# Optimization experiments

Measured on AMD Instinct MI355X. Metric: run time of the kernel, lower is better.

Reference implementation:

```python
import jax, jax.numpy as jnp
import numpy as np

H = 128      # hidden_size
ATT = 128    # attention_size
NS = 1024    # num attendee statements
NE = 512     # num attendee eres
M = 1024     # num attenders


def setup_inputs() -> dict:
    key = jax.random.key(0)
    ks = jax.random.split(key, 16)
    s = 1.0 / np.sqrt(H)
    return {
        'attendee_stmts': jax.random.normal(ks[0], (NS, H), jnp.float32),
        'attendee_eres': jax.random.normal(ks[1], (NE, H), jnp.float32),
        'attender': jax.random.normal(ks[2], (M, H), jnp.float32),
        # Score stmt_to_stmt (concat): Linear(2H->H) then Linear(H->1)
        'Wc_s': jax.random.normal(ks[3], (H, 2 * H), jnp.float32) * s,
        'bc_s': jax.random.normal(ks[4], (H,), jnp.float32) * s,
        'ws_s': jax.random.normal(ks[5], (H,), jnp.float32) * s,
        'bs_s': jax.random.normal(ks[6], (1,), jnp.float32) * s,
        # Score ere_to_stmt (concat)
        'Wc_e': jax.random.normal(ks[7], (H, 2 * H), jnp.float32) * s,
        'bc_e': jax.random.normal(ks[8], (H,), jnp.float32) * s,
        'ws_e': jax.random.normal(ks[9], (H,), jnp.float32) * s,
        'bs_e': jax.random.normal(ks[10], (1,), jnp.float32) * s,
        # Attention combine: Linear(3H -> ATT)
        'W_lin': jax.random.normal(ks[11], (ATT, 3 * H), jnp.float32) * s,
        'b_lin': jax.random.normal(ks[12], (ATT,), jnp.float32) * s,
        # coherence_linear: Linear(ATT -> 1)
        'W_coh': jax.random.normal(ks[13], (1, ATT), jnp.float32) * s,
        'b_coh': jax.random.normal(ks[14], (1,), jnp.float32) * s,
    }


def _concat_score(first, second, Wc, bc, ws, bs):
    # torch: single(tanh(concat(cat([first_i, second_j])))) over all (i, j)
    # split concat weight so we never materialize the [N, M, 2H] concat
    h = first.shape[-1]
    A = first @ Wc[:, :h].T + bc          # [N, H]
    B = second @ Wc[:, h:].T              # [M, H]
    Hnm = jnp.tanh(A[:, None, :] + B[None, :, :])   # [N, M, H]
    return jnp.einsum('nmh,h->nm', Hnm, ws) + bs[0]  # [N, M]


def reference(attendee_stmts, attendee_eres, attender,
              Wc_s, bc_s, ws_s, bs_s,
              Wc_e, bc_e, ws_e, bs_e,
              W_lin, b_lin, W_coh, b_coh):
    # unnormalized scores, softmax over attendees (dim 0)
    w_ss = jax.nn.softmax(_concat_score(attendee_stmts, attender, Wc_s, bc_s, ws_s, bs_s), axis=0)  # [NS, M]
    w_es = jax.nn.softmax(_concat_score(attendee_eres, attender, Wc_e, bc_e, ws_e, bs_e), axis=0)   # [NE, M]
    # context vectors: weights^T @ attendees
    ctx_s = jnp.einsum('nm,nh->mh', w_ss, attendee_stmts)  # [M, H]
    ctx_e = jnp.einsum('nm,nh->mh', w_es, attendee_eres)   # [M, H]
    feats = jnp.concatenate([attender, ctx_s, ctx_e], axis=-1)  # [M, 3H]
    att_vec = jnp.tanh(feats @ W_lin.T + b_lin)                 # [M, ATT]
    coherence = att_vec @ W_coh.T + b_coh                       # [M, 1]
    return coherence
```

## Files before the change

### kernel.cpp

```cpp
#include <hip/hip_runtime.h>
#include <math.h>

#define H   128
#define NS  1024
#define NE  512
#define M   1024
#define K2  2.8853900817779268f

__device__ __forceinline__ float exp2_fast(float x) {
#if __has_builtin(__builtin_amdgcn_exp2f)
    return __builtin_amdgcn_exp2f(x);
#else
    return __expf(x * 0.6931471805599453f);
#endif
}

__device__ __forceinline__ float fast_tanh(float x) {
    float e = __expf(2.0f * x);
    float r = __builtin_amdgcn_rcpf(1.0f + e);
    return 1.0f - 2.0f * r;
}

__global__ __launch_bounds__(256) void k_tr(const float* __restrict__ Wc_s,
                                            const float* __restrict__ Wc_e,
                                            const float* __restrict__ W_lin,
                                            float* __restrict__ WT_s1, float* __restrict__ WT_s2,
                                            float* __restrict__ WT_e1, float* __restrict__ WT_e2,
                                            float* __restrict__ WT_lin) {
    int idx = blockIdx.x * 256 + threadIdx.x;
    if (idx < 65536) {
        int t = idx >> 14, r = idx & 16383, k = r >> 7, hh = r & 127;
        const float* src = (t < 2) ? Wc_s : Wc_e;
        int off = (t & 1) * H;
        float v = K2 * src[hh * 256 + off + k];
        float* dst = (t == 0) ? WT_s1 : (t == 1) ? WT_s2 : (t == 2) ? WT_e1 : WT_e2;
        dst[r] = v;
    } else {
        int j2 = idx - 65536;
        int k = j2 >> 7, a = j2 & 127;
        WT_lin[j2] = W_lin[a * 384 + k];
    }
}

__global__ __launch_bounds__(256) void k_proj(const float* __restrict__ stmts,
                                              const float* __restrict__ eres,
                                              const float* __restrict__ attender,
                                              const float* __restrict__ WT_s1,
                                              const float* __restrict__ WT_s2,
                                              const float* __restrict__ WT_e1,
                                              const float* __restrict__ WT_e2,
                                              const float* __restrict__ bc_s,
                                              const float* __restrict__ bc_e,
                                              float* __restrict__ EAT_s, float* __restrict__ EB_s,
                                              float* __restrict__ EAT_e, float* __restrict__ EB_e) {
    __shared__ float xr[16][H];
    __shared__ float red[16][H];
    int b   = blockIdx.x;
    int tid = threadIdx.x;
    int t    = tid & 127;
    int half = tid >> 7;

    if (b < 96) {
        const float *X, *WT, *bias; float* OT; int r0, N;
        if (b < 64) { X = stmts; WT = WT_s1; bias = bc_s; OT = EAT_s; r0 = b * 16;        N = NS; }
        else        { X = eres;  WT = WT_e1; bias = bc_e; OT = EAT_e; r0 = (b - 64) * 16; N = NE; }
        for (int i = tid; i < 16 * H; i += 256) xr[i >> 7][i & 127] = X[(r0 + (i >> 7)) * H + (i & 127)];
        __syncthreads();
        float b0 = (half == 0) ? K2 * bias[t] : 0.0f;
        float acc[16];
        #pragma unroll
        for (int r = 0; r < 16; ++r) acc[r] = b0;
        int k0 = half * 64;
        #pragma unroll 4
        for (int k = k0; k < k0 + 64; ++k) {
            float wv = WT[k * H + t];
            #pragma unroll
            for (int r = 0; r < 16; ++r) acc[r] += xr[r][k] * wv;
        }
        if (half) {
            #pragma unroll
            for (int r = 0; r < 16; ++r) red[r][t] = acc[r];
        }
        __syncthreads();
        if (!half) {
            #pragma unroll
            for (int r = 0; r < 16; ++r) xr[r][t] = exp2_fast(acc[r] + red[r][t]);
        }
        __syncthreads();
        {
            int hh  = tid >> 1;
            int seg = (tid & 1) * 8;
            float4 v0 = make_float4(xr[seg + 0][hh], xr[seg + 1][hh], xr[seg + 2][hh], xr[seg + 3][hh]);
            float4 v1 = make_float4(xr[seg + 4][hh], xr[seg + 5][hh], xr[seg + 6][hh], xr[seg + 7][hh]);
            *(float4*)(OT + (size_t)hh * N + r0 + seg)     = v0;
            *(float4*)(OT + (size_t)hh * N + r0 + seg + 4) = v1;
        }
    } else {
        int b2 = b - 96;
        const float* WT = (b2 < 256) ? WT_s2 : WT_e2;
        float* O        = (b2 < 256) ? EB_s : EB_e;
        int r0          = (b2 & 255) * 4;
        float* xf = &xr[0][0];
        xf[tid]       = attender[r0 * H + tid];
        xf[tid + 256] = attender[r0 * H + 256 + tid];
        __syncthreads();
        float acc[4] = {0.f, 0.f, 0.f, 0.f};
        int k0 = half * 64;
        #pragma unroll 8
        for (int k = k0; k < k0 + 64; ++k) {
            float wv = WT[k * H + t];
            #pragma unroll
            for (int r = 0; r < 4; ++r) acc[r] += xf[r * H + k] * wv;
        }
        if (half) {
            #pragma unroll
            for (int r = 0; r < 4; ++r) red[r][t] = acc[r];
        }
        __syncthreads();
        if (!half) {
            #pragma unroll
            for (int r = 0; r < 4; ++r) O[(r0 + r) * H + t] = exp2_fast(acc[r] + red[r][t]);
        }
    }
}

#define PAIR(eax, eay, ebx, eby, wx, wy, accv)                 \
    { float q0 = fmaf(eax, ebx, 1.0f);                         \
      float q1 = fmaf(eay, eby, 1.0f);                         \
      float nn = wx * q1; nn = fmaf(wy, q0, nn);               \
      float rr = __builtin_amdgcn_rcpf(q0 * q1);               \
      accv = fmaf(nn, rr, accv); }

__global__ __launch_bounds__(512, 4) void k_score_ctx(const float* __restrict__ EAT_s,
                                                      const float* __restrict__ EB_s,
                                                      const float* __restrict__ ws_s,
                                                      const float* __restrict__ EAT_e,
                                                      const float* __restrict__ EB_e,
                                                      const float* __restrict__ ws_e,
                                                      const float* __restrict__ stmts,
                                                      const float* __restrict__ eres,
                                                      float* __restrict__ ctx_s,
                                                      float* __restrict__ ctx_e) {
    __shared__ float Bs[4][H];
    __shared__ float wbuf[1024][4];
    __shared__ float part[4][4][H];
    __shared__ float scrm[8][4], scrs[8][4], rzl[4];

    int b = blockIdx.x;
    bool is_e = (b >= 256);
    int m0 = (is_e ? (b - 256) : b) * 4;
    const float* EAT = is_e ? EAT_e : EAT_s;
    const float* EB  = is_e ? EB_e  : EB_s;
    const float* wsv = is_e ? ws_e  : ws_s;
    const float* X   = is_e ? eres  : stmts;
    float* ctxout    = is_e ? ctx_e : ctx_s;
    int N    = is_e ? NE : NS;
    int ROWS = is_e ? 1 : 2;
    int t = threadIdx.x;

    Bs[t >> 7][t & 127] = EB[(size_t)(m0 + (t >> 7)) * H + (t & 127)];
    __syncthreads();

    float acc[2][4] = {{0.f,0.f,0.f,0.f},{0.f,0.f,0.f,0.f}};
    float a[2][8];
    #pragma unroll
    for (int k = 0; k < 8; ++k) a[0][k] = EAT[(size_t)k * N + t];
    if (ROWS > 1) {
        #pragma unroll
        for (int k = 0; k < 8; ++k) a[1][k] = EAT[(size_t)k * N + t + 512];
    }
    #pragma unroll
    for (int ch = 0; ch < 16; ++ch) {
        int h0 = ch * 8;
        float an[2][8];
        if (ch < 15) {
            #pragma unroll
            for (int k = 0; k < 8; ++k) an[0][k] = EAT[(size_t)(h0 + 8 + k) * N + t];
            if (ROWS > 1) {
                #pragma unroll
                for (int k = 0; k < 8; ++k) an[1][k] = EAT[(size_t)(h0 + 8 + k) * N + t + 512];
            }
        }
        float wv[8];
        #pragma unroll
        for (int k = 0; k < 8; ++k) wv[k] = wsv[h0 + k];
        #pragma unroll
        for (int mj = 0; mj < 4; ++mj) {
            float bv[8];
            #pragma unroll
            for (int k = 0; k < 8; ++k) bv[k] = Bs[mj][h0 + k];
            PAIR(a[0][0], a[0][1], bv[0], bv[1], wv[0], wv[1], acc[0][mj]);
            PAIR(a[0][2], a[0][3], bv[2], bv[3], wv[2], wv[3], acc[0][mj]);
            PAIR(a[0][4], a[0][5], bv[4], bv[5], wv[4], wv[5], acc[0][mj]);
            PAIR(a[0][6], a[0][7], bv[6], bv[7], wv[6], wv[7], acc[0][mj]);
            if (ROWS > 1) {
                PAIR(a[1][0], a[1][1], bv[0], bv[1], wv[0], wv[1], acc[1][mj]);
                PAIR(a[1][2], a[1][3], bv[2], bv[3], wv[2], wv[3], acc[1][mj]);
                PAIR(a[1][4], a[1][5], bv[4], bv[5], wv[4], wv[5], acc[1][mj]);
                PAIR(a[1][6], a[1][7], bv[6], bv[7], wv[6], wv[7], acc[1][mj]);
            }
        }
        if (ch < 15) {
            #pragma unroll
            for (int k = 0; k < 8; ++k) a[0][k] = an[0][k];
            if (ROWS > 1) {
                #pragma unroll
                for (int k = 0; k < 8; ++k) a[1][k] = an[1][k];
            }
        }
    }

    int wave = t >> 6;
    float mx[4];
    for (int mj = 0; mj < 4; ++mj) {
        float v = -2.0f * acc[0][mj];
        if (ROWS > 1) v = fmaxf(v, -2.0f * acc[1][mj]);
        mx[mj] = v;
    }
    #pragma unroll
    for (int off = 32; off > 0; off >>= 1)
        for (int mj = 0; mj < 4; ++mj) mx[mj] = fmaxf(mx[mj], __shfl_xor(mx[mj], off, 64));
    if ((t & 63) == 0) {
        for (int mj = 0; mj < 4; ++mj) scrm[wave][mj] = mx[mj];
    }
    __syncthreads();
    for (int mj = 0; mj < 4; ++mj) {
        float r = scrm[0][mj];
        for (int i = 1; i < 8; ++i) r = fmaxf(r, scrm[i][mj]);
        mx[mj] = r;
    }

    float w0[4], w1[4], sm[4];
    for (int mj = 0; mj < 4; ++mj) {
        w0[mj] = __expf(fmaf(-2.0f, acc[0][mj], -mx[mj]));
        sm[mj] = w0[mj];
        if (ROWS > 1) { w1[mj] = __expf(fmaf(-2.0f, acc[1][mj], -mx[mj])); sm[mj] += w1[mj]; }
    }
    #pragma unroll
    for (int off = 32; off > 0; off >>= 1)
        for (int mj = 0; mj < 4; ++mj) sm[mj] += __shfl_xor(sm[mj], off, 64);
    if ((t & 63) == 0) {
        for (int mj = 0; mj < 4; ++mj) scrs[wave][mj] = sm[mj];
    }

    for (int mj = 0; mj < 4; ++mj) {
        wbuf[t][mj] = w0[mj];
        if (ROWS > 1) wbuf[t + 512][mj] = w1[mj];
    }
    __syncthreads();
    if (t < 4) {
        float s = scrs[0][t];
        for (int i = 1; i < 8; ++i) s += scrs[i][t];
        rzl[t] = __builtin_amdgcn_rcpf(s);
    }
    __syncthreads();

    {
        int h = t & 127;
        int g = t >> 7;
        int CH = N >> 2;
        const float* Xb = X + (size_t)(g * CH) * H + h;
        const float* wb = &wbuf[g * CH][0];
        float cacc[4] = {0.f, 0.f, 0.f, 0.f};
        #pragma unroll 8
        for (int nn = 0; nn < CH; ++nn) {
            float x = Xb[(size_t)nn * H];
            float4 w4 = *(const float4*)(wb + nn * 4);
            cacc[0] += w4.x * x; cacc[1] += w4.y * x;
            cacc[2] += w4.z * x; cacc[3] += w4.w * x;
        }
        #pragma unroll
        for (int mj = 0; mj < 4; ++mj) part[g][mj][h] = cacc[mj];
    }
    __syncthreads();
    {
        int mj = t >> 7, h = t & 127;
        float s = part[0][mj][h] + part[1][mj][h] + part[2][mj][h] + part[3][mj][h];
        ctxout[(size_t)(m0 + mj) * H + h] = s * rzl[mj];
    }
}

__global__ __launch_bounds__(512) void k_mlp(const float* __restrict__ attender,
                                             const float* __restrict__ ctx_s,
                                             const float* __restrict__ ctx_e,
                                             const float* __restrict__ WT_lin,
                                             const float* __restrict__ b_lin,
                                             const float* __restrict__ W_coh,
                                             const float* __restrict__ b_coh,
                                             float* __restrict__ out) {
    __shared__ float feats[4][3 * H];
    __shared__ float red2[8];
    int m0 = blockIdx.x * 4;
    int t  = threadIdx.x;

    for (int i = t; i < 4 * 3 * H; i += 512) {
        int r = i / (3 * H), c = i % (3 * H);
        float v;
        if (c < H)            v = attender[(size_t)(m0 + r) * H + c];
        else if (c < 2 * H)   v = ctx_s[(size_t)(m0 + r) * H + (c - H)];
        else                  v = ctx_e[(size_t)(m0 + r) * H + (c - 2 * H)];
        feats[r][c] = v;
    }
    __syncthreads();

    int a  = t & 127;
    int jm = t >> 7;
    float acc = b_lin[a];
    #pragma unroll 8
    for (int k = 0; k < 3 * H; ++k)
        acc += feats[jm][k] * WT_lin[k * H + a];
    float v = fast_tanh(acc) * W_coh[a];
    #pragma unroll
    for (int off = 32; off > 0; off >>= 1) v += __shfl_down(v, off, 64);
    if ((t & 63) == 0) red2[t >> 6] = v;
    __syncthreads();
    if (t < 4) out[m0 + t] = red2[2 * t] + red2[2 * t + 1] + b_coh[0];
}

extern "C" void kernel_launch(void* const* d_in, const int* in_sizes, int n_in,
                              void* d_out, int out_size, void* d_ws, size_t ws_size,
                              hipStream_t stream) {
    const float* stmts    = (const float*)d_in[0];
    const float* eres     = (const float*)d_in[1];
    const float* attender = (const float*)d_in[2];
    const float* Wc_s     = (const float*)d_in[3];
    const float* bc_s     = (const float*)d_in[4];
    const float* ws_s     = (const float*)d_in[5];
    const float* Wc_e     = (const float*)d_in[7];
    const float* bc_e     = (const float*)d_in[8];
    const float* ws_e     = (const float*)d_in[9];
    const float* W_lin    = (const float*)d_in[11];
    const float* b_lin    = (const float*)d_in[12];
    const float* W_coh    = (const float*)d_in[13];
    const float* b_coh    = (const float*)d_in[14];
    float* out = (float*)d_out;

    float* ws    = (float*)d_ws;
    float* WT_s1 = ws;
    float* WT_s2 = WT_s1 + H * H;
    float* WT_e1 = WT_s2 + H * H;
    float* WT_e2 = WT_e1 + H * H;
    float* WT_li = WT_e2 + H * H;
    float* EAT_s = WT_li + 3 * H * H;
    float* EB_s  = EAT_s + NS * H;
    float* EAT_e = EB_s + M * H;
    float* EB_e  = EAT_e + NE * H;
    float* c_s   = EB_e + M * H;
    float* c_e   = c_s + (size_t)M * H;

    k_tr<<<448, 256, 0, stream>>>(Wc_s, Wc_e, W_lin, WT_s1, WT_s2, WT_e1, WT_e2, WT_li);
    k_proj<<<608, 256, 0, stream>>>(stmts, eres, attender, WT_s1, WT_s2, WT_e1, WT_e2,
                                    bc_s, bc_e, EAT_s, EB_s, EAT_e, EB_e);
    k_score_ctx<<<512, 512, 0, stream>>>(EAT_s, EB_s, ws_s, EAT_e, EB_e, ws_e,
                                         stmts, eres, c_s, c_e);
    k_mlp<<<M / 4, 512, 0, stream>>>(attender, c_s, c_e, WT_li, b_lin, W_coh, b_coh, out);
}
```

Measured before the change: 67.88 us.

## Halve attenders per block in score kernel to double grid and occupancy

Each score/context block now handles 2 attenders instead of 4, so the grid grows from 512 to 1024 blocks and the launch bound asks for 8 blocks per CU. The shared-memory staging of the attender projection is removed, and B values are read straight from global memory (uniform loads). The software prefetch of the next EAT chunk is also dropped. The aim is more parallelism and lower register and LDS pressure. In exchange, each EAT element is reloaded twice as often across blocks, and the exp/rcp work per loaded element falls, which lowers arithmetic intensity.

Result: slower. 76.52 us (+12.7%).

```diff
diff --git a/kernel.cpp b/kernel.cpp
--- a/kernel.cpp
+++ b/kernel.cpp
@@ -131,7 +131,7 @@
       float rr = __builtin_amdgcn_rcpf(q0 * q1);               \
       accv = fmaf(nn, rr, accv); }
 
-__global__ __launch_bounds__(512, 4) void k_score_ctx(const float* __restrict__ EAT_s,
+__global__ __launch_bounds__(512, 8) void k_score_ctx(const float* __restrict__ EAT_s,
                                                       const float* __restrict__ EB_s,
                                                       const float* __restrict__ ws_s,
                                                       const float* __restrict__ EAT_e,
@@ -141,14 +141,13 @@
                                                       const float* __restrict__ eres,
                                                       float* __restrict__ ctx_s,
                                                       float* __restrict__ ctx_e) {
-    __shared__ float Bs[4][H];
-    __shared__ float wbuf[1024][4];
-    __shared__ float part[4][4][H];
-    __shared__ float scrm[8][4], scrs[8][4], rzl[4];
+    __shared__ float wbuf[1024][2];
+    __shared__ float part[4][2][H];
+    __shared__ float scrm[8][2], scrs[8][2], rzl[2];
 
     int b = blockIdx.x;
-    bool is_e = (b >= 256);
-    int m0 = (is_e ? (b - 256) : b) * 4;
+    bool is_e = (b >= 512);
+    int m0 = (is_e ? (b - 512) : b) * 2;
     const float* EAT = is_e ? EAT_e : EAT_s;
     const float* EB  = is_e ? EB_e  : EB_s;
     const float* wsv = is_e ? ws_e  : ws_s;
@@ -158,97 +157,84 @@
     int ROWS = is_e ? 1 : 2;
     int t = threadIdx.x;
 
-    Bs[t >> 7][t & 127] = EB[(size_t)(m0 + (t >> 7)) * H + (t & 127)];
-    __syncthreads();
-
-    float acc[2][4] = {{0.f,0.f,0.f,0.f},{0.f,0.f,0.f,0.f}};
-    float a[2][8];
-    #pragma unroll
-    for (int k = 0; k < 8; ++k) a[0][k] = EAT[(size_t)k * N + t];
-    if (ROWS > 1) {
-        #pragma unroll
-        for (int k = 0; k < 8; ++k) a[1][k] = EAT[(size_t)k * N + t + 512];
-    }
-    #pragma unroll
+    const float* eb0 = EB + (size_t)m0 * H;
+    const float* eb1 = EB + (size_t)(m0 + 1) * H;
+
+    float acc[2][2] = {{0.f, 0.f}, {0.f, 0.f}};
     for (int ch = 0; ch < 16; ++ch) {
         int h0 = ch * 8;
-        float an[2][8];
-        if (ch < 15) {
-            #pragma unroll
-            for (int k = 0; k < 8; ++k) an[0][k] = EAT[(size_t)(h0 + 8 + k) * N + t];
-            if (ROWS > 1) {
-                #pragma unroll
-                for (int k = 0; k < 8; ++k) an[1][k] = EAT[(size_t)(h0 + 8 + k) * N + t + 512];
-            }
-        }
-        float wv[8];
+        float a0[8], a1[8];
         #pragma unroll
-        for (int k = 0; k < 8; ++k) wv[k] = wsv[h0 + k];
+        for (int k = 0; k < 8; ++k) a0[k] = EAT[(size_t)(h0 + k) * N + t];
+        if (ROWS > 1) {
+            #pragma unroll
+            for (int k = 0; k < 8; ++k) a1[k] = EAT[(size_t)(h0 + k) * N + t + 512];
+        }
+        float wv[8], b0[8], b1[8];
         #pragma unroll
-        for (int mj = 0; mj < 4; ++mj) {
-            float bv[8];
-            #pragma unroll
-            for (int k = 0; k < 8; ++k) bv[k] = Bs[mj][h0 + k];
-            PAIR(a[0][0], a[0][1], bv[0], bv[1], wv[0], wv[1], acc[0][mj]);
-            PAIR(a[0][2], a[0][3], bv[2], bv[3], wv[2], wv[3], acc[0][mj]);
-            PAIR(a[0][4], a[0][5], bv[4], bv[5], wv[4], wv[5], acc[0][mj]);
-            PAIR(a[0][6], a[0][7], bv[6], bv[7], wv[6], wv[7], acc[0][mj]);
-            if (ROWS > 1) {
-                PAIR(a[1][0], a[1][1], bv[0], bv[1], wv[0], wv[1], acc[1][mj]);
-                PAIR(a[1][2], a[1][3], bv[2], bv[3], wv[2], wv[3], acc[1][mj]);
-                PAIR(a[1][4], a[1][5], bv[4], bv[5], wv[4], wv[5], acc[1][mj]);
-                PAIR(a[1][6], a[1][7], bv[6], bv[7], wv[6], wv[7], acc[1][mj]);
-            }
-        }
-        if (ch < 15) {
-            #pragma unroll
-            for (int k = 0; k < 8; ++k) a[0][k] = an[0][k];
-            if (ROWS > 1) {
-                #pragma unroll
-                for (int k = 0; k < 8; ++k) a[1][k] = an[1][k];
-            }
+        for (int k = 0; k < 8; ++k) {
+            wv[k] = wsv[h0 + k];
+            b0[k] = eb0[h0 + k];
+            b1[k] = eb1[h0 + k];
+        }
+        PAIR(a0[0], a0[1], b0[0], b0[1], wv[0], wv[1], acc[0][0]);
+        PAIR(a0[2], a0[3], b0[2], b0[3], wv[2], wv[3], acc[0][0]);
+        PAIR(a0[4], a0[5], b0[4], b0[5], wv[4], wv[5], acc[0][0]);
+        PAIR(a0[6], a0[7], b0[6], b0[7], wv[6], wv[7], acc[0][0]);
+        PAIR(a0[0], a0[1], b1[0], b1[1], wv[0], wv[1], acc[0][1]);
+        PAIR(a0[2], a0[3], b1[2], b1[3], wv[2], wv[3], acc[0][1]);
+        PAIR(a0[4], a0[5], b1[4], b1[5], wv[4], wv[5], acc[0][1]);
+        PAIR(a0[6], a0[7], b1[6], b1[7], wv[6], wv[7], acc[0][1]);
+        if (ROWS > 1) {
+            PAIR(a1[0], a1[1], b0[0], b0[1], wv[0], wv[1], acc[1][0]);
+            PAIR(a1[2], a1[3], b0[2], b0[3], wv[2], wv[3], acc[1][0]);
+            PAIR(a1[4], a1[5], b0[4], b0[5], wv[4], wv[5], acc[1][0]);
+            PAIR(a1[6], a1[7], b0[6], b0[7], wv[6], wv[7], acc[1][0]);
+            PAIR(a1[0], a1[1], b1[0], b1[1], wv[0], wv[1], acc[1][1]);
+            PAIR(a1[2], a1[3], b1[2], b1[3], wv[2], wv[3], acc[1][1]);
+            PAIR(a1[4], a1[5], b1[4], b1[5], wv[4], wv[5], acc[1][1]);
+            PAIR(a1[6], a1[7], b1[6], b1[7], wv[6], wv[7], acc[1][1]);
         }
     }
 
     int wave = t >> 6;
-    float mx[4];
-    for (int mj = 0; mj < 4; ++mj) {
+    float mx[2];
+    for (int mj = 0; mj < 2; ++mj) {
         float v = -2.0f * acc[0][mj];
         if (ROWS > 1) v = fmaxf(v, -2.0f * acc[1][mj]);
         mx[mj] = v;
     }
     #pragma unroll
     for (int off = 32; off > 0; off >>= 1)
-        for (int mj = 0; mj < 4; ++mj) mx[mj] = fmaxf(mx[mj], __shfl_xor(mx[mj], off, 64));
+        for (int mj = 0; mj < 2; ++mj) mx[mj] = fmaxf(mx[mj], __shfl_xor(mx[mj], off, 64));
     if ((t & 63) == 0) {
-        for (int mj = 0; mj < 4; ++mj) scrm[wave][mj] = mx[mj];
-    }
-    __syncthreads();
-    for (int mj = 0; mj < 4; ++mj) {
+        for (int mj = 0; mj < 2; ++mj) scrm[wave][mj] = mx[mj];
+    }
+    __syncthreads();
+    for (int mj = 0; mj < 2; ++mj) {
         float r = scrm[0][mj];
         for (int i = 1; i < 8; ++i) r = fmaxf(r, scrm[i][mj]);
         mx[mj] = r;
     }
 
-    float w0[4], w1[4], sm[4];
-    for (int mj = 0; mj < 4; ++mj) {
+    float w0[2], w1[2], sm[2];
+    for (int mj = 0; mj < 2; ++mj) {
         w0[mj] = __expf(fmaf(-2.0f, acc[0][mj], -mx[mj]));
         sm[mj] = w0[mj];
         if (ROWS > 1) { w1[mj] = __expf(fmaf(-2.0f, acc[1][mj], -mx[mj])); sm[mj] += w1[mj]; }
     }
     #pragma unroll
     for (int off = 32; off > 0; off >>= 1)
-        for (int mj = 0; mj < 4; ++mj) sm[mj] += __shfl_xor(sm[mj], off, 64);
+        for (int mj = 0; mj < 2; ++mj) sm[mj] += __shfl_xor(sm[mj], off, 64);
     if ((t & 63) == 0) {
-        for (int mj = 0; mj < 4; ++mj) scrs[wave][mj] = sm[mj];
-    }
-
-    for (int mj = 0; mj < 4; ++mj) {
-        wbuf[t][mj] = w0[mj];
-        if (ROWS > 1) wbuf[t + 512][mj] = w1[mj];
-    }
-    __syncthreads();
-    if (t < 4) {
+        for (int mj = 0; mj < 2; ++mj) scrs[wave][mj] = sm[mj];
+    }
+
+    wbuf[t][0] = w0[0];
+    wbuf[t][1] = w0[1];
+    if (ROWS > 1) { wbuf[t + 512][0] = w1[0]; wbuf[t + 512][1] = w1[1]; }
+    __syncthreads();
+    if (t < 2) {
         float s = scrs[0][t];
         for (int i = 1; i < 8; ++i) s += scrs[i][t];
         rzl[t] = __builtin_amdgcn_rcpf(s);
@@ -261,19 +247,19 @@
         int CH = N >> 2;
         const float* Xb = X + (size_t)(g * CH) * H + h;
         const float* wb = &wbuf[g * CH][0];
-        float cacc[4] = {0.f, 0.f, 0.f, 0.f};
+        float c0 = 0.f, c1 = 0.f;
         #pragma unroll 8
         for (int nn = 0; nn < CH; ++nn) {
             float x = Xb[(size_t)nn * H];
-            float4 w4 = *(const float4*)(wb + nn * 4);
-            cacc[0] += w4.x * x; cacc[1] += w4.y * x;
-            cacc[2] += w4.z * x; cacc[3] += w4.w * x;
-        }
-        #pragma unroll
-        for (int mj = 0; mj < 4; ++mj) part[g][mj][h] = cacc[mj];
-    }
-    __syncthreads();
-    {
+            float2 w2 = *(const float2*)(wb + nn * 2);
+            c0 += w2.x * x;
+            c1 += w2.y * x;
+        }
+        part[g][0][h] = c0;
+        part[g][1][h] = c1;
+    }
+    __syncthreads();
+    if (t < 2 * H) {
         int mj = t >> 7, h = t & 127;
         float s = part[0][mj][h] + part[1][mj][h] + part[2][mj][h] + part[3][mj][h];
         ctxout[(size_t)(m0 + mj) * H + h] = s * rzl[mj];
@@ -351,7 +337,7 @@
     k_tr<<<448, 256, 0, stream>>>(Wc_s, Wc_e, W_lin, WT_s1, WT_s2, WT_e1, WT_e2, WT_li);
     k_proj<<<608, 256, 0, stream>>>(stmts, eres, attender, WT_s1, WT_s2, WT_e1, WT_e2,
                                     bc_s, bc_e, EAT_s, EB_s, EAT_e, EB_e);
-    k_score_ctx<<<512, 512, 0, stream>>>(EAT_s, EB_s, ws_s, EAT_e, EB_e, ws_e,
-                                         stmts, eres, c_s, c_e);
+    k_score_ctx<<<1024, 512, 0, stream>>>(EAT_s, EB_s, ws_s, EAT_e, EB_e, ws_e,
+                                          stmts, eres, c_s, c_e);
     k_mlp<<<M / 4, 512, 0, stream>>>(attender, c_s, c_e, WT_li, b_lin, W_coh, b_coh, out);
 }
```

## Split score hidden dim across two thread halves with vectorized attendee loads

Applied to the files above, without the earlier changes.

Restructures the score phase so each thread handles several consecutive attendees (4 for stmts, 2 for eres) over half of the hidden dimension, using vector loads of the transposed A matrix. The two halves' partial scores are combined through a padded shared buffer before the softmax. B values are now read directly from global memory instead of being staged in shared memory. The intent is to balance work between the stmt and ere blocks and cut per-element load instructions. The cost is an extra shared-memory reduction and sync, plus only half the threads doing the softmax.

Result: faster. 65.62 us (-3.3%).

```diff
diff --git a/kernel.cpp b/kernel.cpp
--- a/kernel.cpp
+++ b/kernel.cpp
@@ -6,6 +6,9 @@
 #define NE  512
 #define M   1024
 #define K2  2.8853900817779268f
+
+typedef float v4 __attribute__((ext_vector_type(4)));
+typedef float v2 __attribute__((ext_vector_type(2)));
 
 __device__ __forceinline__ float exp2_fast(float x) {
 #if __has_builtin(__builtin_amdgcn_exp2f)
@@ -141,10 +144,10 @@
                                                       const float* __restrict__ eres,
                                                       float* __restrict__ ctx_s,
                                                       float* __restrict__ ctx_e) {
-    __shared__ float Bs[4][H];
+    __shared__ float partial[16][257];
     __shared__ float wbuf[1024][4];
     __shared__ float part[4][4][H];
-    __shared__ float scrm[8][4], scrs[8][4], rzl[4];
+    __shared__ float scrm[4][4], scrs[4][4], rzl[4];
 
     int b = blockIdx.x;
     bool is_e = (b >= 256);
@@ -154,105 +157,131 @@
     const float* wsv = is_e ? ws_e  : ws_s;
     const float* X   = is_e ? eres  : stmts;
     float* ctxout    = is_e ? ctx_e : ctx_s;
-    int N    = is_e ? NE : NS;
-    int ROWS = is_e ? 1 : 2;
-    int t = threadIdx.x;
-
-    Bs[t >> 7][t & 127] = EB[(size_t)(m0 + (t >> 7)) * H + (t & 127)];
-    __syncthreads();
-
-    float acc[2][4] = {{0.f,0.f,0.f,0.f},{0.f,0.f,0.f,0.f}};
-    float a[2][8];
-    #pragma unroll
-    for (int k = 0; k < 8; ++k) a[0][k] = EAT[(size_t)k * N + t];
-    if (ROWS > 1) {
-        #pragma unroll
-        for (int k = 0; k < 8; ++k) a[1][k] = EAT[(size_t)k * N + t + 512];
-    }
-    #pragma unroll
-    for (int ch = 0; ch < 16; ++ch) {
-        int h0 = ch * 8;
-        float an[2][8];
-        if (ch < 15) {
-            #pragma unroll
-            for (int k = 0; k < 8; ++k) an[0][k] = EAT[(size_t)(h0 + 8 + k) * N + t];
-            if (ROWS > 1) {
+    int N  = is_e ? NE : NS;
+    int NL = is_e ? 2 : 4;
+    int t  = threadIdx.x;
+    int tq = t & 255;
+    int hg = t >> 8;
+    int hbase = hg * 64;
+
+    float acc[4][4] = {{0.f,0.f,0.f,0.f},{0.f,0.f,0.f,0.f},
+                       {0.f,0.f,0.f,0.f},{0.f,0.f,0.f,0.f}};
+
+    if (!is_e) {
+        const float* base = EAT + 4 * tq;
+        v4 a[4], an[4];
+        #pragma unroll
+        for (int k = 0; k < 4; ++k) a[k] = *(const v4*)(base + (size_t)(hbase + k) * NS);
+        for (int ch = 0; ch < 16; ++ch) {
+            int h0 = hbase + ch * 4;
+            if (ch < 15) {
                 #pragma unroll
-                for (int k = 0; k < 8; ++k) an[1][k] = EAT[(size_t)(h0 + 8 + k) * N + t + 512];
-            }
-        }
-        float wv[8];
-        #pragma unroll
-        for (int k = 0; k < 8; ++k) wv[k] = wsv[h0 + k];
-        #pragma unroll
-        for (int mj = 0; mj < 4; ++mj) {
-            float bv[8];
-            #pragma unroll
-            for (int k = 0; k < 8; ++k) bv[k] = Bs[mj][h0 + k];
-            PAIR(a[0][0], a[0][1], bv[0], bv[1], wv[0], wv[1], acc[0][mj]);
-            PAIR(a[0][2], a[0][3], bv[2], bv[3], wv[2], wv[3], acc[0][mj]);
-            PAIR(a[0][4], a[0][5], bv[4], bv[5], wv[4], wv[5], acc[0][mj]);
-            PAIR(a[0][6], a[0][7], bv[6], bv[7], wv[6], wv[7], acc[0][mj]);
-            if (ROWS > 1) {
-                PAIR(a[1][0], a[1][1], bv[0], bv[1], wv[0], wv[1], acc[1][mj]);
-                PAIR(a[1][2], a[1][3], bv[2], bv[3], wv[2], wv[3], acc[1][mj]);
-                PAIR(a[1][4], a[1][5], bv[4], bv[5], wv[4], wv[5], acc[1][mj]);
-                PAIR(a[1][6], a[1][7], bv[6], bv[7], wv[6], wv[7], acc[1][mj]);
-            }
-        }
-        if (ch < 15) {
-            #pragma unroll
-            for (int k = 0; k < 8; ++k) a[0][k] = an[0][k];
-            if (ROWS > 1) {
+                for (int k = 0; k < 4; ++k)
+                    an[k] = *(const v4*)(base + (size_t)(h0 + 4 + k) * NS);
+            }
+            float wv[4];
+            #pragma unroll
+            for (int k = 0; k < 4; ++k) wv[k] = wsv[h0 + k];
+            #pragma unroll
+            for (int mj = 0; mj < 4; ++mj) {
+                float b0 = EB[(size_t)(m0 + mj) * H + h0 + 0];
+                float b1 = EB[(size_t)(m0 + mj) * H + h0 + 1];
+                float b2 = EB[(size_t)(m0 + mj) * H + h0 + 2];
+                float b3 = EB[(size_t)(m0 + mj) * H + h0 + 3];
                 #pragma unroll
-                for (int k = 0; k < 8; ++k) a[1][k] = an[1][k];
-            }
-        }
-    }
-
+                for (int i = 0; i < 4; ++i) {
+                    PAIR(a[0][i], a[1][i], b0, b1, wv[0], wv[1], acc[i][mj]);
+                    PAIR(a[2][i], a[3][i], b2, b3, wv[2], wv[3], acc[i][mj]);
+                }
+            }
+            #pragma unroll
+            for (int k = 0; k < 4; ++k) a[k] = an[k];
+        }
+    } else {
+        const float* base = EAT + 2 * tq;
+        v2 a[4], an[4];
+        #pragma unroll
+        for (int k = 0; k < 4; ++k) a[k] = *(const v2*)(base + (size_t)(hbase + k) * NE);
+        for (int ch = 0; ch < 16; ++ch) {
+            int h0 = hbase + ch * 4;
+            if (ch < 15) {
+                #pragma unroll
+                for (int k = 0; k < 4; ++k)
+                    an[k] = *(const v2*)(base + (size_t)(h0 + 4 + k) * NE);
+            }
+            float wv[4];
+            #pragma unroll
+            for (int k = 0; k < 4; ++k) wv[k] = wsv[h0 + k];
+            #pragma unroll
+            for (int mj = 0; mj < 4; ++mj) {
+                float b0 = EB[(size_t)(m0 + mj) * H + h0 + 0];
+                float b1 = EB[(size_t)(m0 + mj) * H + h0 + 1];
+                float b2 = EB[(size_t)(m0 + mj) * H + h0 + 2];
+                float b3 = EB[(size_t)(m0 + mj) * H + h0 + 3];
+                #pragma unroll
+                for (int i = 0; i < 2; ++i) {
+                    PAIR(a[0][i], a[1][i], b0, b1, wv[0], wv[1], acc[i][mj]);
+                    PAIR(a[2][i], a[3][i], b2, b3, wv[2], wv[3], acc[i][mj]);
+                }
+            }
+            #pragma unroll
+            for (int k = 0; k < 4; ++k) a[k] = an[k];
+        }
+    }
+
+    if (hg) {
+        for (int i = 0; i < NL; ++i)
+            #pragma unroll
+            for (int j = 0; j < 4; ++j) partial[i * 4 + j][tq] = acc[i][j];
+    }
+    __syncthreads();
     int wave = t >> 6;
-    float mx[4];
-    for (int mj = 0; mj < 4; ++mj) {
-        float v = -2.0f * acc[0][mj];
-        if (ROWS > 1) v = fmaxf(v, -2.0f * acc[1][mj]);
-        mx[mj] = v;
-    }
-    #pragma unroll
-    for (int off = 32; off > 0; off >>= 1)
-        for (int mj = 0; mj < 4; ++mj) mx[mj] = fmaxf(mx[mj], __shfl_xor(mx[mj], off, 64));
-    if ((t & 63) == 0) {
-        for (int mj = 0; mj < 4; ++mj) scrm[wave][mj] = mx[mj];
-    }
-    __syncthreads();
-    for (int mj = 0; mj < 4; ++mj) {
-        float r = scrm[0][mj];
-        for (int i = 1; i < 8; ++i) r = fmaxf(r, scrm[i][mj]);
-        mx[mj] = r;
-    }
-
-    float w0[4], w1[4], sm[4];
-    for (int mj = 0; mj < 4; ++mj) {
-        w0[mj] = __expf(fmaf(-2.0f, acc[0][mj], -mx[mj]));
-        sm[mj] = w0[mj];
-        if (ROWS > 1) { w1[mj] = __expf(fmaf(-2.0f, acc[1][mj], -mx[mj])); sm[mj] += w1[mj]; }
-    }
-    #pragma unroll
-    for (int off = 32; off > 0; off >>= 1)
-        for (int mj = 0; mj < 4; ++mj) sm[mj] += __shfl_xor(sm[mj], off, 64);
-    if ((t & 63) == 0) {
-        for (int mj = 0; mj < 4; ++mj) scrs[wave][mj] = sm[mj];
-    }
-
-    for (int mj = 0; mj < 4; ++mj) {
-        wbuf[t][mj] = w0[mj];
-        if (ROWS > 1) wbuf[t + 512][mj] = w1[mj];
-    }
-    __syncthreads();
-    if (t < 4) {
-        float s = scrs[0][t];
-        for (int i = 1; i < 8; ++i) s += scrs[i][t];
-        rzl[t] = __builtin_amdgcn_rcpf(s);
-    }
+    if (!hg) {
+        for (int i = 0; i < NL; ++i)
+            #pragma unroll
+            for (int j = 0; j < 4; ++j) acc[i][j] += partial[i * 4 + j][tq];
+        float mx[4];
+        #pragma unroll
+        for (int j = 0; j < 4; ++j) {
+            float v = -2.0f * acc[0][j];
+            for (int i = 1; i < NL; ++i) v = fmaxf(v, -2.0f * acc[i][j]);
+            mx[j] = v;
+        }
+        #pragma unroll
+        for (int off = 32; off > 0; off >>= 1)
+            for (int j = 0; j < 4; ++j) mx[j] = fmaxf(mx[j], __shfl_xor(mx[j], off, 64));
+        if ((t & 63) == 0) {
+            for (int j = 0; j < 4; ++j) scrm[wave][j] = mx[j];
+        }
+    }
+    __syncthreads();
+    if (!hg) {
+        float mx[4], sm[4];
+        #pragma unroll
+        for (int j = 0; j < 4; ++j)
+            mx[j] = fmaxf(fmaxf(scrm[0][j], scrm[1][j]), fmaxf(scrm[2][j], scrm[3][j]));
+        #pragma unroll
+        for (int j = 0; j < 4; ++j) sm[j] = 0.f;
+        float w[4][4];
+        for (int i = 0; i < NL; ++i) {
+            #pragma unroll
+            for (int j = 0; j < 4; ++j) {
+                w[i][j] = __expf(fmaf(-2.0f, acc[i][j], -mx[j]));
+                sm[j] += w[i][j];
+            }
+        }
+        #pragma unroll
+        for (int off = 32; off > 0; off >>= 1)
+            for (int j = 0; j < 4; ++j) sm[j] += __shfl_xor(sm[j], off, 64);
+        if ((t & 63) == 0) {
+            for (int j = 0; j < 4; ++j) scrs[wave][j] = sm[j];
+        }
+        for (int i = 0; i < NL; ++i)
+            *(v4*)&wbuf[NL * tq + i][0] = (v4){w[i][0], w[i][1], w[i][2], w[i][3]};
+    }
+    __syncthreads();
+    if (t < 4)
+        rzl[t] = __builtin_amdgcn_rcpf(scrs[0][t] + scrs[1][t] + scrs[2][t] + scrs[3][t]);
     __syncthreads();
 
     {
@@ -261,16 +290,16 @@
         int CH = N >> 2;
         const float* Xb = X + (size_t)(g * CH) * H + h;
         const float* wb = &wbuf[g * CH][0];
-        float cacc[4] = {0.f, 0.f, 0.f, 0.f};
+        float c[4] = {0.f, 0.f, 0.f, 0.f};
         #pragma unroll 8
         for (int nn = 0; nn < CH; ++nn) {
             float x = Xb[(size_t)nn * H];
             float4 w4 = *(const float4*)(wb + nn * 4);
-            cacc[0] += w4.x * x; cacc[1] += w4.y * x;
-            cacc[2] += w4.z * x; cacc[3] += w4.w * x;
-        }
-        #pragma unroll
-        for (int mj = 0; mj < 4; ++mj) part[g][mj][h] = cacc[mj];
+            c[0] += w4.x * x; c[1] += w4.y * x;
+            c[2] += w4.z * x; c[3] += w4.w * x;
+        }
+        #pragma unroll
+        for (int mj = 0; mj < 4; ++mj) part[g][mj][h] = c[mj];
     }
     __syncthreads();
     {
```
